# Optimization experiments

Measured on AMD Instinct MI355X. Metric: run time of the kernel, lower is better.

Reference implementation:

```python
import jax, jax.numpy as jnp
import numpy as np

CHUNK = 128  # intra-chunk causal block size for the chunked linear-attention scan


def setup_inputs() -> dict:
    key = jax.random.key(0)
    ks = jax.random.split(key, 7)
    B, H, N, D, F = 1, 24, 4096, 128, 256
    q = jax.random.normal(ks[0], (B, H, N, D), dtype=jnp.float32)
    k = jax.random.normal(ks[1], (B, H, N, D), dtype=jnp.float32)
    v = jax.random.normal(ks[2], (B, H, N, D), dtype=jnp.float32)
    # fan-in scaling so phi features / accumulated state stay numerically sane
    w1 = jax.random.normal(ks[3], (F, D), dtype=jnp.float32) * (D ** -0.5)
    b1 = jax.random.normal(ks[4], (F,), dtype=jnp.float32) * 0.02
    w2 = jax.random.normal(ks[5], (F, F), dtype=jnp.float32) * (F ** -0.5)
    b2 = jax.random.normal(ks[6], (F,), dtype=jnp.float32) * 0.02
    return {"q": q, "k": k, "v": v, "w1": w1, "b1": b1, "w2": w2, "b2": b2}


def _phi(x, w1, b1, w2, b2):
    # Linear(D->F) -> SiLU -> Linear(F->F)
    h = jax.nn.silu(jnp.einsum('bnd,fd->bnf', x, w1) + b1)
    return jnp.einsum('bnf,gf->bng', h, w2) + b2


def _causal_scan(qp, kp, vf):
    # out_t = q_t . (sum_{s<=t} k_s v_s^T) / (t+1), chunked parallel form.
    BH, N, F = qp.shape
    D = vf.shape[-1]
    C = CHUNK
    nC = N // C
    qc = qp.reshape(BH, nC, C, F).transpose(1, 0, 2, 3)  # [nC,BH,C,F]
    kc = kp.reshape(BH, nC, C, F).transpose(1, 0, 2, 3)
    vc = vf.reshape(BH, nC, C, D).transpose(1, 0, 2, 3)
    offsets = (jnp.arange(nC) * C).astype(qp.dtype)
    mask = jnp.tril(jnp.ones((C, C), dtype=qp.dtype))  # include diagonal
    pos = jnp.arange(1, C + 1, dtype=qp.dtype)

    def step(w, inp):
        qb, kb, vb, off = inp
        inter = jnp.einsum('bcf,bfd->bcd', qb, w)
        attn = jnp.einsum('bcf,bsf->bcs', qb, kb) * mask
        intra = jnp.einsum('bcs,bsd->bcd', attn, vb)
        counts = off + pos  # global (token_idx + 1)
        out = (inter + intra) / counts[None, :, None]
        w = w + jnp.einsum('bcf,bcd->bfd', kb, vb)
        return w, out

    w0 = jnp.zeros((BH, F, D), dtype=qp.dtype)
    _, outs = jax.lax.scan(step, w0, (qc, kc, vc, offsets))  # outs [nC,BH,C,D]
    return outs.transpose(1, 0, 2, 3).reshape(BH, N, D)


def reference(q, k, v, w1, b1, w2, b2):
    B, H, N, D = q.shape
    qf = q.reshape(B * H, N, D)
    kf = k.reshape(B * H, N, D)
    vf = v.reshape(B * H, N, D)
    qp = _phi(qf, w1, b1, w2, b2)
    kp = _phi(kf, w1, b1, w2, b2)
    out_fwd = _causal_scan(qp, kp, vf)
    out_rev = _causal_scan(qp[:, ::-1], kp[:, ::-1], vf[:, ::-1])[:, ::-1]
    return (out_fwd + out_rev).reshape(B, H, N, D)
```

## Files before the change

kernel.cpp:

```cpp
#include <hip/hip_runtime.h>


typedef __attribute__((ext_vector_type(8))) _Float16 f16x8;
typedef __attribute__((ext_vector_type(4))) _Float16 f16x4;
typedef __attribute__((ext_vector_type(4))) float f32x4;

#define MFMA16(a, b, c) __builtin_amdgcn_mfma_f32_16x16x32_f16((a), (b), (c), 0, 0, 0)

constexpr int BH   = 24;
constexpr int NSEQ = 4096;
constexpr int DD   = 128;
constexpr int FF   = 256;
constexpr int CHK  = 128;
constexpr int NC   = NSEQ / CHK;
constexpr int NROWS = BH * NSEQ;

__global__ void prep_kernel(const float* __restrict__ w1, const float* __restrict__ w2,
                            _Float16* __restrict__ w1h, _Float16* __restrict__ w2h) {
  int i = blockIdx.x * 256 + threadIdx.x;
  if (i < FF * DD) w1h[i] = (_Float16)w1[i];
  if (i < FF * FF) w2h[i] = (_Float16)w2[i];
}

__global__ __launch_bounds__(256, 2)
void phi_kernel(const float* __restrict__ q, const float* __restrict__ k,
                const float* __restrict__ b1, const float* __restrict__ b2,
                const _Float16* __restrict__ w1h, const _Float16* __restrict__ w2h,
                _Float16* __restrict__ qp, _Float16* __restrict__ kp) {
  __shared__ __align__(16) _Float16 xs[64][136];
  __shared__ __align__(16) _Float16 hs[64][264];
  int blk = blockIdx.x;
  const float* src;
  _Float16* dst;
  int rb;
  if (blk < NROWS / 64) { src = q; dst = qp; rb = blk * 64; }
  else                  { src = k; dst = kp; rb = (blk - NROWS / 64) * 64; }
  int tid = threadIdx.x;
  int lane = tid & 63, wv = tid >> 6;
  int wm = wv & 1, wn = wv >> 1;
  int lr = lane & 15, lq = lane >> 4;

  f16x8 b1r[4][8];
#pragma unroll
  for (int ks = 0; ks < 4; ++ks)
#pragma unroll
    for (int fn = 0; fn < 8; ++fn)
      b1r[ks][fn] = *(const f16x8*)&w1h[(wn * 128 + fn * 16 + lr) * DD + ks * 32 + lq * 8];

#pragma unroll
  for (int i = 0; i < 8; ++i) {
    int flat = i * 1024 + tid * 4;
    int r = flat >> 7, c = flat & 127;
    float4 xv = *(const float4*)&src[(size_t)(rb + r) * DD + c];
    f16x4 hv = {(_Float16)xv.x, (_Float16)xv.y, (_Float16)xv.z, (_Float16)xv.w};
    *(f16x4*)&xs[r][c] = hv;
  }
  __syncthreads();

  f32x4 acc[2][8] = {};
#pragma unroll
  for (int ks = 0; ks < 4; ++ks) {
    f16x8 av[2];
#pragma unroll
    for (int im = 0; im < 2; ++im)
      av[im] = *(const f16x8*)&xs[wm * 32 + im * 16 + lr][ks * 32 + lq * 8];
#pragma unroll
    for (int fn = 0; fn < 8; ++fn)
#pragma unroll
      for (int im = 0; im < 2; ++im) acc[im][fn] = MFMA16(av[im], b1r[ks][fn], acc[im][fn]);
  }

  f16x8 b2r[8][4];
#pragma unroll
  for (int ks = 0; ks < 8; ++ks)
#pragma unroll
    for (int fn = 0; fn < 4; ++fn)
      b2r[ks][fn] = *(const f16x8*)&w2h[(wn * 128 + fn * 16 + lr) * FF + ks * 32 + lq * 8];

#pragma unroll
  for (int im = 0; im < 2; ++im)
#pragma unroll
    for (int fn = 0; fn < 8; ++fn) {
      int f = wn * 128 + fn * 16 + lr;
      float bb = b1[f];
      int r0 = wm * 32 + im * 16 + lq * 4;
#pragma unroll
      for (int r = 0; r < 4; ++r) {
        float xv = acc[im][fn][r] + bb;
        float sv = xv / (1.0f + __expf(-xv));
        hs[r0 + r][f] = (_Float16)sv;
      }
    }
  __syncthreads();

  f16x8 b3r[8][4];
  f32x4 ac2[2][4] = {};
#pragma unroll
  for (int ks = 0; ks < 8; ++ks) {
    f16x8 av[2];
#pragma unroll
    for (int im = 0; im < 2; ++im)
      av[im] = *(const f16x8*)&hs[wm * 32 + im * 16 + lr][ks * 32 + lq * 8];
#pragma unroll
    for (int fn = 0; fn < 4; ++fn)
#pragma unroll
      for (int im = 0; im < 2; ++im) ac2[im][fn] = MFMA16(av[im], b2r[ks][fn], ac2[im][fn]);
#pragma unroll
    for (int fn = 0; fn < 4; ++fn)
      b3r[ks][fn] = *(const f16x8*)&w2h[(wn * 128 + (4 + fn) * 16 + lr) * FF + ks * 32 + lq * 8];
  }
#pragma unroll
  for (int im = 0; im < 2; ++im)
#pragma unroll
    for (int fn = 0; fn < 4; ++fn) {
      int g = wn * 128 + fn * 16 + lr;
      float bb = b2[g];
      int r0 = wm * 32 + im * 16 + lq * 4;
#pragma unroll
      for (int r = 0; r < 4; ++r)
        dst[(size_t)(rb + r0 + r) * FF + g] = (_Float16)(ac2[im][fn][r] + bb);
    }

  f32x4 ac3[2][4] = {};
#pragma unroll
  for (int ks = 0; ks < 8; ++ks) {
    f16x8 av[2];
#pragma unroll
    for (int im = 0; im < 2; ++im)
      av[im] = *(const f16x8*)&hs[wm * 32 + im * 16 + lr][ks * 32 + lq * 8];
#pragma unroll
    for (int fn = 0; fn < 4; ++fn)
#pragma unroll
      for (int im = 0; im < 2; ++im) ac3[im][fn] = MFMA16(av[im], b3r[ks][fn], ac3[im][fn]);
  }
#pragma unroll
  for (int im = 0; im < 2; ++im)
#pragma unroll
    for (int fn = 0; fn < 4; ++fn) {
      int g = wn * 128 + (4 + fn) * 16 + lr;
      float bb = b2[g];
      int r0 = wm * 32 + im * 16 + lq * 4;
#pragma unroll
      for (int r = 0; r < 4; ++r)
        dst[(size_t)(rb + r0 + r) * FF + g] = (_Float16)(ac3[im][fn][r] + bb);
    }
}

__global__ void s_kernel(const float* __restrict__ v, const _Float16* __restrict__ kp,
                         _Float16* __restrict__ S) {
  __shared__ __align__(16) _Float16 vt[64][136];
  __shared__ __align__(16) _Float16 kt[128][136];
  int b = blockIdx.x;
  int fh = b & 1, dh = (b >> 1) & 1, c = (b >> 2) & 31, bh = b >> 7;
  const float*    vc  = v  + ((size_t)bh * NSEQ + c * CHK) * DD;
  const _Float16* kpc = kp + ((size_t)bh * NSEQ + c * CHK) * FF;
  int tid = threadIdx.x;
  for (int i = tid; i < 128 * 64; i += 256) {
    int s = i >> 6, d = i & 63;
    vt[d][s] = (_Float16)vc[(size_t)s * DD + dh * 64 + d];
  }
  for (int i = tid; i < 128 * 128; i += 256) {
    int s = i >> 7, f = i & 127;
    kt[f][s] = kpc[(size_t)s * FF + fh * 128 + f];
  }
  __syncthreads();
  int lane = tid & 63, wv = tid >> 6, wm = wv & 1, wn = wv >> 1;
  int lr = lane & 15, lq = lane >> 4;
  f32x4 acc[2][4] = {};
#pragma unroll
  for (int ks = 0; ks < 4; ++ks) {
    f16x8 av[2];
#pragma unroll
    for (int im = 0; im < 2; ++im)
      av[im] = *(const f16x8*)&vt[wm * 32 + im * 16 + lr][ks * 32 + lq * 8];
#pragma unroll
    for (int j = 0; j < 4; ++j) {
      f16x8 bv = *(const f16x8*)&kt[wn * 64 + j * 16 + lr][ks * 32 + lq * 8];
#pragma unroll
      for (int im = 0; im < 2; ++im) acc[im][j] = MFMA16(av[im], bv, acc[im][j]);
    }
  }
  _Float16* Sp = S + ((size_t)bh * NC + c) * (size_t)(DD * FF);
#pragma unroll
  for (int im = 0; im < 2; ++im)
#pragma unroll
    for (int j = 0; j < 4; ++j) {
      int f = fh * 128 + wn * 64 + j * 16 + lr;
#pragma unroll
      for (int r = 0; r < 4; ++r) {
        int d = dh * 64 + wm * 32 + im * 16 + lq * 4 + r;
        Sp[(size_t)d * FF + f] = (_Float16)acc[im][j][r];
      }
    }
}

__global__ void prefix_kernel(const _Float16* __restrict__ S, _Float16* __restrict__ Wf,
                              _Float16* __restrict__ Wr) {
  size_t idx = (size_t)blockIdx.x * 256 + threadIdx.x;
  int bh = (int)(idx >> 15);
  int df = (int)(idx & 32767);
  size_t base = (size_t)bh * NC * 32768 + df;
  float vals[NC];
#pragma unroll
  for (int c = 0; c < NC; ++c) vals[c] = (float)S[base + (size_t)c * 32768];
  float run = 0.f;
#pragma unroll
  for (int c = 0; c < NC; ++c) { Wf[base + (size_t)c * 32768] = (_Float16)run; run += vals[c]; }
  run = 0.f;
#pragma unroll
  for (int c = NC - 1; c >= 0; --c) { Wr[base + (size_t)c * 32768] = (_Float16)run; run += vals[c]; }
}

__global__ __launch_bounds__(256, 2)
void scan_kernel(const _Float16* __restrict__ qp, const _Float16* __restrict__ kp,
                 const float* __restrict__ v, const _Float16* __restrict__ Wf,
                 const _Float16* __restrict__ Wr, float* __restrict__ out) {
  __shared__ __align__(16) _Float16 vt[128][136];
  __shared__ __align__(16) _Float16 P[64][136];
  int b = blockIdx.x;
  int ih = b & 1, c = (b >> 1) & 31, bh = b >> 6;
  const _Float16* qpc = qp + ((size_t)bh * NSEQ + c * CHK) * FF;
  const _Float16* kpc = kp + ((size_t)bh * NSEQ + c * CHK) * FF;
  const float*    vc  = v  + ((size_t)bh * NSEQ + c * CHK) * DD;
  int tid = threadIdx.x;
  int lane = tid & 63, wv = tid >> 6, wm = wv & 1, wn = wv >> 1;
  int lr = lane & 15, lq = lane >> 4;

  f16x8 aq[2][8];
#pragma unroll
  for (int im = 0; im < 2; ++im)
#pragma unroll
    for (int ks = 0; ks < 8; ++ks)
      aq[im][ks] = *(const f16x8*)&qpc[(size_t)(ih * 64 + wm * 32 + im * 16 + lr) * FF + ks * 32 + lq * 8];

  f16x8 bk[8][4];
#pragma unroll
  for (int ks = 0; ks < 8; ++ks)
#pragma unroll
    for (int j = 0; j < 4; ++j)
      bk[ks][j] = *(const f16x8*)&kpc[(size_t)(wn * 64 + j * 16 + lr) * FF + ks * 32 + lq * 8];

  for (int i = tid; i < CHK * DD; i += 256) {
    int s = i >> 7, d = i & 127;
    vt[d][s] = (_Float16)vc[i];
  }

  f32x4 pacc[2][4] = {};
#pragma unroll
  for (int ks = 0; ks < 8; ++ks)
#pragma unroll
    for (int j = 0; j < 4; ++j)
#pragma unroll
      for (int im = 0; im < 2; ++im) pacc[im][j] = MFMA16(aq[im][ks], bk[ks][j], pacc[im][j]);
#pragma unroll
  for (int im = 0; im < 2; ++im)
#pragma unroll
    for (int j = 0; j < 4; ++j)
#pragma unroll
      for (int r = 0; r < 4; ++r)
        P[wm * 32 + im * 16 + lq * 4 + r][wn * 64 + j * 16 + lr] = (_Float16)pacc[im][j][r];

  const _Float16* Wfc = Wf + ((size_t)bh * NC + c) * (size_t)(DD * FF);
  const _Float16* Wrc = Wr + ((size_t)bh * NC + c) * (size_t)(DD * FF);

  f16x8 bf[8], br[8];
#pragma unroll
  for (int ks = 0; ks < 8; ++ks) {
    int d = wn * 64 + 0 * 16 + lr;
    bf[ks] = *(const f16x8*)&Wfc[(size_t)d * FF + ks * 32 + lq * 8];
    br[ks] = *(const f16x8*)&Wrc[(size_t)d * FF + ks * 32 + lq * 8];
  }
  __syncthreads();

  f32x4 af[2][4] = {}, ar[2][4] = {};
#pragma unroll
  for (int j = 0; j < 4; ++j) {
#pragma unroll
    for (int ks = 0; ks < 8; ++ks)
#pragma unroll
      for (int im = 0; im < 2; ++im) {
        af[im][j] = MFMA16(aq[im][ks], bf[ks], af[im][j]);
        ar[im][j] = MFMA16(aq[im][ks], br[ks], ar[im][j]);
      }
    if (j < 3) {
#pragma unroll
      for (int ks = 0; ks < 8; ++ks) {
        int d = wn * 64 + (j + 1) * 16 + lr;
        bf[ks] = *(const f16x8*)&Wfc[(size_t)d * FF + ks * 32 + lq * 8];
        br[ks] = *(const f16x8*)&Wrc[(size_t)d * FF + ks * 32 + lq * 8];
      }
    }
    {
      int ks = j;
#pragma unroll
      for (int im = 0; im < 2; ++im) {
        int irow = wm * 32 + im * 16 + lr;
        int ichunk = ih * 64 + irow;
        f16x8 p = *(const f16x8*)&P[irow][ks * 32 + lq * 8];
        f16x8 pf = p, pr = p;
#pragma unroll
        for (int jj = 0; jj < 8; ++jj) {
          int s = ks * 32 + lq * 8 + jj;
          pf[jj] = (s <= ichunk) ? p[jj] : (_Float16)0.0f;
          pr[jj] = (s >= ichunk) ? p[jj] : (_Float16)0.0f;
        }
#pragma unroll
        for (int jd = 0; jd < 4; ++jd) {
          f16x8 bv = *(const f16x8*)&vt[wn * 64 + jd * 16 + lr][ks * 32 + lq * 8];
          af[im][jd] = MFMA16(pf, bv, af[im][jd]);
          ar[im][jd] = MFMA16(pr, bv, ar[im][jd]);
        }
      }
    }
  }

  float* oc = out + ((size_t)bh * NSEQ + c * CHK) * DD;
#pragma unroll
  for (int im = 0; im < 2; ++im)
#pragma unroll
    for (int j = 0; j < 4; ++j) {
      int d = wn * 64 + j * 16 + lr;
#pragma unroll
      for (int r = 0; r < 4; ++r) {
        int il = ih * 64 + wm * 32 + im * 16 + lq * 4 + r;
        int gi = c * CHK + il;
        float val = af[im][j][r] / (float)(gi + 1) + ar[im][j][r] / (float)(NSEQ - gi);
        oc[(size_t)il * DD + d] = val;
      }
    }
}

extern "C" void kernel_launch(void* const* d_in, const int* in_sizes, int n_in,
                              void* d_out, int out_size, void* d_ws, size_t ws_size,
                              hipStream_t stream) {
  const float* q  = (const float*)d_in[0];
  const float* k  = (const float*)d_in[1];
  const float* v  = (const float*)d_in[2];
  const float* w1 = (const float*)d_in[3];
  const float* b1 = (const float*)d_in[4];
  const float* w2 = (const float*)d_in[5];
  const float* b2 = (const float*)d_in[6];
  float* out = (float*)d_out;

  char* ws = (char*)d_ws;
  const size_t SZ = 50331648ull;
  _Float16* w1h = (_Float16*)(ws);
  _Float16* w2h = (_Float16*)(ws + 65536);
  _Float16* qp  = (_Float16*)(ws + 196608);
  _Float16* kp  = (_Float16*)(ws + 196608 + SZ);
  _Float16* S   = (_Float16*)(ws + 196608 + 2 * SZ);
  _Float16* Wf  = (_Float16*)(ws + 196608 + 3 * SZ);
  _Float16* Wr  = (_Float16*)(ws + 196608 + 4 * SZ);

  prep_kernel<<<dim3(256), dim3(256), 0, stream>>>(w1, w2, w1h, w2h);
  phi_kernel<<<dim3(2 * NROWS / 64), dim3(256), 0, stream>>>(q, k, b1, b2, w1h, w2h, qp, kp);
  s_kernel<<<dim3(BH * NC * 4), dim3(256), 0, stream>>>(v, kp, S);
  prefix_kernel<<<dim3(BH * DD * FF / 256), dim3(256), 0, stream>>>(S, Wf, Wr);
  scan_kernel<<<dim3(BH * NC * 2), dim3(256), 0, stream>>>(qp, kp, v, Wf, Wr, out);
}
```

Measured before the change: 482.9 us.

## Restructure pipeline with pre-transposed V and K features and larger tiles

```diff
diff --git a/kernel.cpp b/kernel.cpp
--- a/kernel.cpp
+++ b/kernel.cpp
@@ -22,236 +22,271 @@
   if (i < FF * FF) w2h[i] = (_Float16)w2[i];
 }
 
-__global__ __launch_bounds__(256, 2)
+__global__ void vt_kernel(const float* __restrict__ v, _Float16* __restrict__ vT) {
+  __shared__ __align__(16) _Float16 lt[128][136];
+  int blk = blockIdx.x;
+  int c = blk & 31, bh = blk >> 5;
+  const float* vc = v + ((size_t)bh * NSEQ + c * CHK) * DD;
+  int tid = threadIdx.x;
+#pragma unroll
+  for (int it = 0; it < 16; ++it) {
+    int flat = it * 1024 + tid * 4;
+    int s = flat >> 7, d0 = flat & 127;
+    float4 xv = *(const float4*)&vc[(size_t)s * DD + d0];
+    lt[d0 + 0][s] = (_Float16)xv.x;
+    lt[d0 + 1][s] = (_Float16)xv.y;
+    lt[d0 + 2][s] = (_Float16)xv.z;
+    lt[d0 + 3][s] = (_Float16)xv.w;
+  }
+  __syncthreads();
+#pragma unroll
+  for (int it = 0; it < 8; ++it) {
+    int flat = it * 256 + tid;
+    int d = flat >> 4, sg = flat & 15;
+    *(f16x8*)&vT[((size_t)bh * DD + d) * NSEQ + c * CHK + sg * 8] =
+        *(const f16x8*)&lt[d][sg * 8];
+  }
+}
+
+__global__ __launch_bounds__(512, 2)
 void phi_kernel(const float* __restrict__ q, const float* __restrict__ k,
                 const float* __restrict__ b1, const float* __restrict__ b2,
                 const _Float16* __restrict__ w1h, const _Float16* __restrict__ w2h,
-                _Float16* __restrict__ qp, _Float16* __restrict__ kp) {
-  __shared__ __align__(16) _Float16 xs[64][136];
-  __shared__ __align__(16) _Float16 hs[64][264];
+                _Float16* __restrict__ qp, _Float16* __restrict__ kp,
+                _Float16* __restrict__ kpT) {
+  __shared__ __align__(16) char smem[137216];
+  _Float16 (*xs)[136]  = (_Float16(*)[136])smem;
+  _Float16 (*w1s)[136] = (_Float16(*)[136])(smem + 34816);
+  _Float16 (*hs)[264]  = (_Float16(*)[264])smem;
+  _Float16 (*w2s)[136] = (_Float16(*)[136])(smem + 67584);
   int blk = blockIdx.x;
   const float* src;
   _Float16* dst;
+  bool isk;
   int rb;
-  if (blk < NROWS / 64) { src = q; dst = qp; rb = blk * 64; }
-  else                  { src = k; dst = kp; rb = (blk - NROWS / 64) * 64; }
+  if (blk < NROWS / 128) { src = q; dst = qp; rb = blk * 128; isk = false; }
+  else                   { src = k; dst = kp; rb = (blk - NROWS / 128) * 128; isk = true; }
   int tid = threadIdx.x;
-  int lane = tid & 63, wv = tid >> 6;
-  int wm = wv & 1, wn = wv >> 1;
-  int lr = lane & 15, lq = lane >> 4;
-
-  f16x8 b1r[4][8];
-#pragma unroll
-  for (int ks = 0; ks < 4; ++ks)
-#pragma unroll
-    for (int fn = 0; fn < 8; ++fn)
-      b1r[ks][fn] = *(const f16x8*)&w1h[(wn * 128 + fn * 16 + lr) * DD + ks * 32 + lq * 8];
-
-#pragma unroll
-  for (int i = 0; i < 8; ++i) {
-    int flat = i * 1024 + tid * 4;
-    int r = flat >> 7, c = flat & 127;
-    float4 xv = *(const float4*)&src[(size_t)(rb + r) * DD + c];
+  int lane = tid & 63, wv = tid >> 6, lr = lane & 15, lq = lane >> 4;
+
+#pragma unroll
+  for (int it = 0; it < 8; ++it) {
+    int flat = it * 512 + tid;
+    int f = flat >> 4, cg = flat & 15;
+    *(f16x8*)&w1s[f][cg * 8] = *(const f16x8*)&w1h[f * DD + cg * 8];
+  }
+#pragma unroll
+  for (int it = 0; it < 8; ++it) {
+    int flat = it * 512 + tid;
+    int r = flat >> 5, dg = flat & 31;
+    float4 xv = *(const float4*)&src[(size_t)(rb + r) * DD + dg * 4];
     f16x4 hv = {(_Float16)xv.x, (_Float16)xv.y, (_Float16)xv.z, (_Float16)xv.w};
-    *(f16x4*)&xs[r][c] = hv;
-  }
-  __syncthreads();
-
-  f32x4 acc[2][8] = {};
+    *(f16x4*)&xs[r][dg * 4] = hv;
+  }
+  __syncthreads();
+
+  int wm1 = wv & 1, wn1 = wv >> 1;
+  f32x4 acc[4][4] = {};
 #pragma unroll
   for (int ks = 0; ks < 4; ++ks) {
-    f16x8 av[2];
-#pragma unroll
-    for (int im = 0; im < 2; ++im)
-      av[im] = *(const f16x8*)&xs[wm * 32 + im * 16 + lr][ks * 32 + lq * 8];
-#pragma unroll
-    for (int fn = 0; fn < 8; ++fn)
-#pragma unroll
-      for (int im = 0; im < 2; ++im) acc[im][fn] = MFMA16(av[im], b1r[ks][fn], acc[im][fn]);
-  }
-
-  f16x8 b2r[8][4];
-#pragma unroll
-  for (int ks = 0; ks < 8; ++ks)
-#pragma unroll
-    for (int fn = 0; fn < 4; ++fn)
-      b2r[ks][fn] = *(const f16x8*)&w2h[(wn * 128 + fn * 16 + lr) * FF + ks * 32 + lq * 8];
-
-#pragma unroll
-  for (int im = 0; im < 2; ++im)
-#pragma unroll
-    for (int fn = 0; fn < 8; ++fn) {
-      int f = wn * 128 + fn * 16 + lr;
+    f16x8 av[4];
+#pragma unroll
+    for (int im = 0; im < 4; ++im)
+      av[im] = *(const f16x8*)&xs[wm1 * 64 + im * 16 + lr][ks * 32 + lq * 8];
+#pragma unroll
+    for (int fn = 0; fn < 4; ++fn) {
+      f16x8 bv = *(const f16x8*)&w1s[wn1 * 64 + fn * 16 + lr][ks * 32 + lq * 8];
+#pragma unroll
+      for (int im = 0; im < 4; ++im) acc[im][fn] = MFMA16(av[im], bv, acc[im][fn]);
+    }
+  }
+  __syncthreads();
+
+#pragma unroll
+  for (int it = 0; it < 8; ++it) {
+    int flat = it * 512 + tid;
+    int g = flat >> 4, cg = flat & 15;
+    *(f16x8*)&w2s[g][cg * 8] = *(const f16x8*)&w2h[(size_t)g * FF + cg * 8];
+  }
+#pragma unroll
+  for (int im = 0; im < 4; ++im)
+#pragma unroll
+    for (int fn = 0; fn < 4; ++fn) {
+      int f = wn1 * 64 + fn * 16 + lr;
       float bb = b1[f];
-      int r0 = wm * 32 + im * 16 + lq * 4;
+      int r0 = wm1 * 64 + im * 16 + lq * 4;
 #pragma unroll
       for (int r = 0; r < 4; ++r) {
         float xv = acc[im][fn][r] + bb;
-        float sv = xv / (1.0f + __expf(-xv));
-        hs[r0 + r][f] = (_Float16)sv;
-      }
-    }
-  __syncthreads();
-
-  f16x8 b3r[8][4];
-  f32x4 ac2[2][4] = {};
-#pragma unroll
-  for (int ks = 0; ks < 8; ++ks) {
-    f16x8 av[2];
-#pragma unroll
-    for (int im = 0; im < 2; ++im)
-      av[im] = *(const f16x8*)&hs[wm * 32 + im * 16 + lr][ks * 32 + lq * 8];
-#pragma unroll
-    for (int fn = 0; fn < 4; ++fn)
-#pragma unroll
-      for (int im = 0; im < 2; ++im) ac2[im][fn] = MFMA16(av[im], b2r[ks][fn], ac2[im][fn]);
-#pragma unroll
-    for (int fn = 0; fn < 4; ++fn)
-      b3r[ks][fn] = *(const f16x8*)&w2h[(wn * 128 + (4 + fn) * 16 + lr) * FF + ks * 32 + lq * 8];
-  }
-#pragma unroll
-  for (int im = 0; im < 2; ++im)
-#pragma unroll
-    for (int fn = 0; fn < 4; ++fn) {
-      int g = wn * 128 + fn * 16 + lr;
+        hs[r0 + r][f] = (_Float16)(xv / (1.0f + __expf(-xv)));
+      }
+    }
+  __syncthreads();
+
+  int wmg = wv & 1, wng = wv >> 1;
+  f32x4 ac2[4][4] = {};
+#pragma unroll
+  for (int ks = 0; ks < 4; ++ks) {
+    f16x8 av[4];
+#pragma unroll
+    for (int im = 0; im < 4; ++im)
+      av[im] = *(const f16x8*)&hs[wmg * 64 + im * 16 + lr][ks * 32 + lq * 8];
+#pragma unroll
+    for (int fn = 0; fn < 4; ++fn) {
+      f16x8 bv = *(const f16x8*)&w2s[wng * 64 + fn * 16 + lr][ks * 32 + lq * 8];
+#pragma unroll
+      for (int im = 0; im < 4; ++im) ac2[im][fn] = MFMA16(av[im], bv, ac2[im][fn]);
+    }
+  }
+  __syncthreads();
+#pragma unroll
+  for (int it = 0; it < 8; ++it) {
+    int flat = it * 512 + tid;
+    int g = flat >> 4, cg = flat & 15;
+    *(f16x8*)&w2s[g][cg * 8] = *(const f16x8*)&w2h[(size_t)g * FF + 128 + cg * 8];
+  }
+  __syncthreads();
+#pragma unroll
+  for (int ks = 0; ks < 4; ++ks) {
+    f16x8 av[4];
+#pragma unroll
+    for (int im = 0; im < 4; ++im)
+      av[im] = *(const f16x8*)&hs[wmg * 64 + im * 16 + lr][128 + ks * 32 + lq * 8];
+#pragma unroll
+    for (int fn = 0; fn < 4; ++fn) {
+      f16x8 bv = *(const f16x8*)&w2s[wng * 64 + fn * 16 + lr][ks * 32 + lq * 8];
+#pragma unroll
+      for (int im = 0; im < 4; ++im) ac2[im][fn] = MFMA16(av[im], bv, ac2[im][fn]);
+    }
+  }
+
+  int bh = rb >> 12, s0 = rb & 4095;
+#pragma unroll
+  for (int im = 0; im < 4; ++im)
+#pragma unroll
+    for (int fn = 0; fn < 4; ++fn) {
+      int g = wng * 64 + fn * 16 + lr;
       float bb = b2[g];
-      int r0 = wm * 32 + im * 16 + lq * 4;
-#pragma unroll
-      for (int r = 0; r < 4; ++r)
-        dst[(size_t)(rb + r0 + r) * FF + g] = (_Float16)(ac2[im][fn][r] + bb);
-    }
-
-  f32x4 ac3[2][4] = {};
-#pragma unroll
-  for (int ks = 0; ks < 8; ++ks) {
-    f16x8 av[2];
-#pragma unroll
-    for (int im = 0; im < 2; ++im)
-      av[im] = *(const f16x8*)&hs[wm * 32 + im * 16 + lr][ks * 32 + lq * 8];
-#pragma unroll
-    for (int fn = 0; fn < 4; ++fn)
-#pragma unroll
-      for (int im = 0; im < 2; ++im) ac3[im][fn] = MFMA16(av[im], b3r[ks][fn], ac3[im][fn]);
-  }
-#pragma unroll
-  for (int im = 0; im < 2; ++im)
-#pragma unroll
-    for (int fn = 0; fn < 4; ++fn) {
-      int g = wn * 128 + (4 + fn) * 16 + lr;
-      float bb = b2[g];
-      int r0 = wm * 32 + im * 16 + lq * 4;
-#pragma unroll
-      for (int r = 0; r < 4; ++r)
-        dst[(size_t)(rb + r0 + r) * FF + g] = (_Float16)(ac3[im][fn][r] + bb);
-    }
-}
-
-__global__ void s_kernel(const float* __restrict__ v, const _Float16* __restrict__ kp,
-                         _Float16* __restrict__ S) {
-  __shared__ __align__(16) _Float16 vt[64][136];
-  __shared__ __align__(16) _Float16 kt[128][136];
-  int b = blockIdx.x;
-  int fh = b & 1, dh = (b >> 1) & 1, c = (b >> 2) & 31, bh = b >> 7;
-  const float*    vc  = v  + ((size_t)bh * NSEQ + c * CHK) * DD;
-  const _Float16* kpc = kp + ((size_t)bh * NSEQ + c * CHK) * FF;
+      int r0 = wmg * 64 + im * 16 + lq * 4;
+#pragma unroll
+      for (int r = 0; r < 4; ++r) {
+        _Float16 val = (_Float16)(ac2[im][fn][r] + bb);
+        dst[(size_t)(rb + r0 + r) * FF + g] = val;
+        if (isk) kpT[((size_t)bh * FF + g) * NSEQ + s0 + r0 + r] = val;
+      }
+    }
+}
+
+__global__ __launch_bounds__(512, 2)
+void s_kernel(const _Float16* __restrict__ vT, const _Float16* __restrict__ kpT,
+              _Float16* __restrict__ S) {
+  __shared__ __align__(16) _Float16 vt[128][136];
+  __shared__ __align__(16) _Float16 kt[256][136];
+  int blk = blockIdx.x;
+  int c = blk & 31, bh = blk >> 5;
   int tid = threadIdx.x;
-  for (int i = tid; i < 128 * 64; i += 256) {
-    int s = i >> 6, d = i & 63;
-    vt[d][s] = (_Float16)vc[(size_t)s * DD + dh * 64 + d];
-  }
-  for (int i = tid; i < 128 * 128; i += 256) {
-    int s = i >> 7, f = i & 127;
-    kt[f][s] = kpc[(size_t)s * FF + fh * 128 + f];
-  }
-  __syncthreads();
-  int lane = tid & 63, wv = tid >> 6, wm = wv & 1, wn = wv >> 1;
-  int lr = lane & 15, lq = lane >> 4;
-  f32x4 acc[2][4] = {};
+#pragma unroll
+  for (int it = 0; it < 4; ++it) {
+    int flat = it * 512 + tid;
+    int d = flat >> 4, sg = flat & 15;
+    *(f16x8*)&vt[d][sg * 8] = *(const f16x8*)&vT[((size_t)bh * DD + d) * NSEQ + c * CHK + sg * 8];
+  }
+#pragma unroll
+  for (int it = 0; it < 8; ++it) {
+    int flat = it * 512 + tid;
+    int f = flat >> 4, sg = flat & 15;
+    *(f16x8*)&kt[f][sg * 8] = *(const f16x8*)&kpT[((size_t)bh * FF + f) * NSEQ + c * CHK + sg * 8];
+  }
+  __syncthreads();
+  int lane = tid & 63, wv = tid >> 6, lr = lane & 15, lq = lane >> 4;
+  int wmd = wv & 1, wnf = wv >> 1;
+  f32x4 acc[4][4] = {};
 #pragma unroll
   for (int ks = 0; ks < 4; ++ks) {
-    f16x8 av[2];
-#pragma unroll
-    for (int im = 0; im < 2; ++im)
-      av[im] = *(const f16x8*)&vt[wm * 32 + im * 16 + lr][ks * 32 + lq * 8];
-#pragma unroll
-    for (int j = 0; j < 4; ++j) {
-      f16x8 bv = *(const f16x8*)&kt[wn * 64 + j * 16 + lr][ks * 32 + lq * 8];
-#pragma unroll
-      for (int im = 0; im < 2; ++im) acc[im][j] = MFMA16(av[im], bv, acc[im][j]);
+    f16x8 av[4];
+#pragma unroll
+    for (int im = 0; im < 4; ++im)
+      av[im] = *(const f16x8*)&vt[wmd * 64 + im * 16 + lr][ks * 32 + lq * 8];
+#pragma unroll
+    for (int fn = 0; fn < 4; ++fn) {
+      f16x8 bv = *(const f16x8*)&kt[wnf * 64 + fn * 16 + lr][ks * 32 + lq * 8];
+#pragma unroll
+      for (int im = 0; im < 4; ++im) acc[im][fn] = MFMA16(av[im], bv, acc[im][fn]);
     }
   }
   _Float16* Sp = S + ((size_t)bh * NC + c) * (size_t)(DD * FF);
 #pragma unroll
-  for (int im = 0; im < 2; ++im)
-#pragma unroll
-    for (int j = 0; j < 4; ++j) {
-      int f = fh * 128 + wn * 64 + j * 16 + lr;
+  for (int im = 0; im < 4; ++im)
+#pragma unroll
+    for (int fn = 0; fn < 4; ++fn) {
+      int f = wnf * 64 + fn * 16 + lr;
 #pragma unroll
       for (int r = 0; r < 4; ++r) {
-        int d = dh * 64 + wm * 32 + im * 16 + lq * 4 + r;
-        Sp[(size_t)d * FF + f] = (_Float16)acc[im][j][r];
-      }
-    }
-}
-
-__global__ void prefix_kernel(const _Float16* __restrict__ S, _Float16* __restrict__ Wf,
-                              _Float16* __restrict__ Wr) {
+        int d = wmd * 64 + im * 16 + lq * 4 + r;
+        Sp[(size_t)d * FF + f] = (_Float16)acc[im][fn][r];
+      }
+    }
+}
+
+__global__ void prefix_kernel(_Float16* S_Wr, _Float16* __restrict__ Wf) {
   size_t idx = (size_t)blockIdx.x * 256 + threadIdx.x;
   int bh = (int)(idx >> 15);
   int df = (int)(idx & 32767);
   size_t base = (size_t)bh * NC * 32768 + df;
   float vals[NC];
 #pragma unroll
-  for (int c = 0; c < NC; ++c) vals[c] = (float)S[base + (size_t)c * 32768];
+  for (int c = 0; c < NC; ++c) vals[c] = (float)S_Wr[base + (size_t)c * 32768];
   float run = 0.f;
 #pragma unroll
   for (int c = 0; c < NC; ++c) { Wf[base + (size_t)c * 32768] = (_Float16)run; run += vals[c]; }
   run = 0.f;
 #pragma unroll
-  for (int c = NC - 1; c >= 0; --c) { Wr[base + (size_t)c * 32768] = (_Float16)run; run += vals[c]; }
-}
-
-__global__ __launch_bounds__(256, 2)
+  for (int c = NC - 1; c >= 0; --c) { S_Wr[base + (size_t)c * 32768] = (_Float16)run; run += vals[c]; }
+}
+
+__global__ __launch_bounds__(512, 2)
 void scan_kernel(const _Float16* __restrict__ qp, const _Float16* __restrict__ kp,
-                 const float* __restrict__ v, const _Float16* __restrict__ Wf,
+                 const _Float16* __restrict__ vT, const _Float16* __restrict__ Wf,
                  const _Float16* __restrict__ Wr, float* __restrict__ out) {
   __shared__ __align__(16) _Float16 vt[128][136];
-  __shared__ __align__(16) _Float16 P[64][136];
-  int b = blockIdx.x;
-  int ih = b & 1, c = (b >> 1) & 31, bh = b >> 6;
+  __shared__ __align__(16) _Float16 P[128][136];
+  int blk = blockIdx.x;
+  int c = blk & 31, bh = blk >> 5;
   const _Float16* qpc = qp + ((size_t)bh * NSEQ + c * CHK) * FF;
   const _Float16* kpc = kp + ((size_t)bh * NSEQ + c * CHK) * FF;
-  const float*    vc  = v  + ((size_t)bh * NSEQ + c * CHK) * DD;
-  int tid = threadIdx.x;
-  int lane = tid & 63, wv = tid >> 6, wm = wv & 1, wn = wv >> 1;
-  int lr = lane & 15, lq = lane >> 4;
+  int tid = threadIdx.x, lane = tid & 63, wv = tid >> 6, lr = lane & 15, lq = lane >> 4;
+  int wm = wv & 3, wn = wv >> 2;
 
   f16x8 aq[2][8];
 #pragma unroll
   for (int im = 0; im < 2; ++im)
 #pragma unroll
     for (int ks = 0; ks < 8; ++ks)
-      aq[im][ks] = *(const f16x8*)&qpc[(size_t)(ih * 64 + wm * 32 + im * 16 + lr) * FF + ks * 32 + lq * 8];
-
-  f16x8 bk[8][4];
+      aq[im][ks] = *(const f16x8*)&qpc[(size_t)(wm * 32 + im * 16 + lr) * FF + ks * 32 + lq * 8];
+#pragma unroll
+  for (int it = 0; it < 4; ++it) {
+    int flat = it * 512 + tid;
+    int d = flat >> 4, sg = flat & 15;
+    *(f16x8*)&vt[d][sg * 8] = *(const f16x8*)&vT[((size_t)bh * DD + d) * NSEQ + c * CHK + sg * 8];
+  }
+  f16x8 bk[2][8];
 #pragma unroll
   for (int ks = 0; ks < 8; ++ks)
-#pragma unroll
-    for (int j = 0; j < 4; ++j)
-      bk[ks][j] = *(const f16x8*)&kpc[(size_t)(wn * 64 + j * 16 + lr) * FF + ks * 32 + lq * 8];
-
-  for (int i = tid; i < CHK * DD; i += 256) {
-    int s = i >> 7, d = i & 127;
-    vt[d][s] = (_Float16)vc[i];
-  }
-
+    bk[0][ks] = *(const f16x8*)&kpc[(size_t)(wn * 64 + lr) * FF + ks * 32 + lq * 8];
   f32x4 pacc[2][4] = {};
 #pragma unroll
-  for (int ks = 0; ks < 8; ++ks)
-#pragma unroll
-    for (int j = 0; j < 4; ++j)
-#pragma unroll
-      for (int im = 0; im < 2; ++im) pacc[im][j] = MFMA16(aq[im][ks], bk[ks][j], pacc[im][j]);
+  for (int j = 0; j < 4; ++j) {
+    int cur = j & 1;
+    if (j < 3)
+#pragma unroll
+      for (int ks = 0; ks < 8; ++ks)
+        bk[cur ^ 1][ks] = *(const f16x8*)&kpc[(size_t)(wn * 64 + (j + 1) * 16 + lr) * FF + ks * 32 + lq * 8];
+#pragma unroll
+    for (int ks = 0; ks < 8; ++ks)
+#pragma unroll
+      for (int im = 0; im < 2; ++im)
+        pacc[im][j] = MFMA16(aq[im][ks], bk[cur][ks], pacc[im][j]);
+  }
 #pragma unroll
   for (int im = 0; im < 2; ++im)
 #pragma unroll
@@ -262,11 +297,10 @@
 
   const _Float16* Wfc = Wf + ((size_t)bh * NC + c) * (size_t)(DD * FF);
   const _Float16* Wrc = Wr + ((size_t)bh * NC + c) * (size_t)(DD * FF);
-
   f16x8 bf[8], br[8];
 #pragma unroll
   for (int ks = 0; ks < 8; ++ks) {
-    int d = wn * 64 + 0 * 16 + lr;
+    int d = wn * 64 + lr;
     bf[ks] = *(const f16x8*)&Wfc[(size_t)d * FF + ks * 32 + lq * 8];
     br[ks] = *(const f16x8*)&Wrc[(size_t)d * FF + ks * 32 + lq * 8];
   }
@@ -274,41 +308,42 @@
 
   f32x4 af[2][4] = {}, ar[2][4] = {};
 #pragma unroll
-  for (int j = 0; j < 4; ++j) {
+  for (int jd = 0; jd < 4; ++jd) {
 #pragma unroll
     for (int ks = 0; ks < 8; ++ks)
 #pragma unroll
       for (int im = 0; im < 2; ++im) {
-        af[im][j] = MFMA16(aq[im][ks], bf[ks], af[im][j]);
-        ar[im][j] = MFMA16(aq[im][ks], br[ks], ar[im][j]);
-      }
-    if (j < 3) {
+        af[im][jd] = MFMA16(aq[im][ks], bf[ks], af[im][jd]);
+        ar[im][jd] = MFMA16(aq[im][ks], br[ks], ar[im][jd]);
+      }
+    if (jd < 3)
 #pragma unroll
       for (int ks = 0; ks < 8; ++ks) {
-        int d = wn * 64 + (j + 1) * 16 + lr;
+        int d = wn * 64 + (jd + 1) * 16 + lr;
         bf[ks] = *(const f16x8*)&Wfc[(size_t)d * FF + ks * 32 + lq * 8];
         br[ks] = *(const f16x8*)&Wrc[(size_t)d * FF + ks * 32 + lq * 8];
       }
-    }
     {
-      int ks = j;
+      int ks = jd;
+      f16x8 bv[4];
+#pragma unroll
+      for (int jd2 = 0; jd2 < 4; ++jd2)
+        bv[jd2] = *(const f16x8*)&vt[wn * 64 + jd2 * 16 + lr][ks * 32 + lq * 8];
 #pragma unroll
       for (int im = 0; im < 2; ++im) {
         int irow = wm * 32 + im * 16 + lr;
-        int ichunk = ih * 64 + irow;
         f16x8 p = *(const f16x8*)&P[irow][ks * 32 + lq * 8];
         f16x8 pf = p, pr = p;
 #pragma unroll
         for (int jj = 0; jj < 8; ++jj) {
           int s = ks * 32 + lq * 8 + jj;
-          pf[jj] = (s <= ichunk) ? p[jj] : (_Float16)0.0f;
-          pr[jj] = (s >= ichunk) ? p[jj] : (_Float16)0.0f;
+          pf[jj] = (s <= irow) ? p[jj] : (_Float16)0.0f;
+          pr[jj] = (s >= irow) ? p[jj] : (_Float16)0.0f;
         }
 #pragma unroll
-        for (int jd = 0; jd < 4; ++jd) {
-          f16x8 bv = *(const f16x8*)&vt[wn * 64 + jd * 16 + lr][ks * 32 + lq * 8];
-          af[im][jd] = MFMA16(pf, bv, af[im][jd]);
-          ar[im][jd] = MFMA16(pr, bv, ar[im][jd]);
+        for (int jd2 = 0; jd2 < 4; ++jd2) {
+          af[im][jd2] = MFMA16(pf, bv[jd2], af[im][jd2]);
+          ar[im][jd2] = MFMA16(pr, bv[jd2], ar[im][jd2]);
         }
       }
     }
@@ -318,14 +353,13 @@
 #pragma unroll
   for (int im = 0; im < 2; ++im)
 #pragma unroll
-    for (int j = 0; j < 4; ++j) {
-      int d = wn * 64 + j * 16 + lr;
+    for (int jd = 0; jd < 4; ++jd) {
+      int d = wn * 64 + jd * 16 + lr;
 #pragma unroll
       for (int r = 0; r < 4; ++r) {
-        int il = ih * 64 + wm * 32 + im * 16 + lq * 4 + r;
+        int il = wm * 32 + im * 16 + lq * 4 + r;
         int gi = c * CHK + il;
-        float val = af[im][j][r] / (float)(gi + 1) + ar[im][j][r] / (float)(NSEQ - gi);
-        oc[(size_t)il * DD + d] = val;
+        oc[(size_t)il * DD + d] = af[im][jd][r] / (float)(gi + 1) + ar[im][jd][r] / (float)(NSEQ - gi);
       }
     }
 }
@@ -348,13 +382,16 @@
   _Float16* w2h = (_Float16*)(ws + 65536);
   _Float16* qp  = (_Float16*)(ws + 196608);
   _Float16* kp  = (_Float16*)(ws + 196608 + SZ);
-  _Float16* S   = (_Float16*)(ws + 196608 + 2 * SZ);
-  _Float16* Wf  = (_Float16*)(ws + 196608 + 3 * SZ);
-  _Float16* Wr  = (_Float16*)(ws + 196608 + 4 * SZ);
+  _Float16* kpT = (_Float16*)(ws + 196608 + 2 * SZ);
+  _Float16* S   = (_Float16*)(ws + 196608 + 3 * SZ);
+  _Float16* vT  = (_Float16*)(ws + 196608 + 4 * SZ);
+  _Float16* Wf  = kpT;
+  _Float16* Wr  = S;
 
   prep_kernel<<<dim3(256), dim3(256), 0, stream>>>(w1, w2, w1h, w2h);
-  phi_kernel<<<dim3(2 * NROWS / 64), dim3(256), 0, stream>>>(q, k, b1, b2, w1h, w2h, qp, kp);
-  s_kernel<<<dim3(BH * NC * 4), dim3(256), 0, stream>>>(v, kp, S);
-  prefix_kernel<<<dim3(BH * DD * FF / 256), dim3(256), 0, stream>>>(S, Wf, Wr);
-  scan_kernel<<<dim3(BH * NC * 2), dim3(256), 0, stream>>>(qp, kp, v, Wf, Wr, out);
-}
+  vt_kernel<<<dim3(BH * NC), dim3(256), 0, stream>>>(v, vT);
+  phi_kernel<<<dim3(2 * NROWS / 128), dim3(512), 0, stream>>>(q, k, b1, b2, w1h, w2h, qp, kp, kpT);
+  s_kernel<<<dim3(BH * NC), dim3(512), 0, stream>>>(vT, kpT, S);
+  prefix_kernel<<<dim3(BH * DD * FF / 256), dim3(256), 0, stream>>>(S, Wf);
+  scan_kernel<<<dim3(BH * NC), dim3(512), 0, stream>>>(qp, kp, vT, Wf, Wr, out);
+}
```

New measurement: 416.0 us. 1.16x faster.
